# Kernel optimization log

Measured on AMD Instinct MI355X. Metric: run time of the kernel, lower is better.

The kernel has to match this reference:

```python
import jax, jax.numpy as jnp
import numpy as np

B = 128      # batch_size
TF = 80      # video_frame (encoder steps)
DEC = 30     # decoder_length
E = 512      # EmbeddingDim / LSTM hidden size
FEAT = 4096  # video feature dim
V = 6000     # total_words (vocab)


def setup_inputs() -> dict:
    key = jax.random.key(0)
    ks = jax.random.split(key, 13)
    s = 0.05  # weight init scale
    d = {
        "feat": jax.random.normal(ks[0], (B, TF, FEAT), jnp.float32),
        "caption": jax.random.normal(ks[1], (B, DEC, E), jnp.float32),
        "caption_one_hot": jax.random.uniform(ks[2], (B, DEC, V), jnp.float32),
        # LSTMCell 1: input 4096 -> hidden 512 (PyTorch gate order i,f,g,o)
        "w_ih1": jax.random.normal(ks[3], (4 * E, FEAT), jnp.float32) * s,
        "w_hh1": jax.random.normal(ks[4], (4 * E, E), jnp.float32) * s,
        "b_ih1": jax.random.normal(ks[5], (4 * E,), jnp.float32) * s,
        "b_hh1": jax.random.normal(ks[6], (4 * E,), jnp.float32) * s,
        # LSTMCell 2: input 2*512 -> hidden 512
        "w_ih2": jax.random.normal(ks[7], (4 * E, 2 * E), jnp.float32) * s,
        "w_hh2": jax.random.normal(ks[8], (4 * E, E), jnp.float32) * s,
        "b_ih2": jax.random.normal(ks[9], (4 * E,), jnp.float32) * s,
        "b_hh2": jax.random.normal(ks[10], (4 * E,), jnp.float32) * s,
        # output projection to vocab
        "w_out": jax.random.normal(ks[11], (V, E), jnp.float32) * s,
        "b_out": jax.random.normal(ks[12], (V,), jnp.float32) * s,
        "keep_rate": 10,  # coin >= keep_rate never true -> teacher forcing
    }
    return d


def _lstm_cell(x, h, c, w_ih, w_hh, b_ih, b_hh):
    # gates: [B, 4E]; PyTorch LSTMCell gate order (i, f, g, o)
    gates = x @ w_ih.T + h @ w_hh.T + b_ih + b_hh
    i, f, g, o = jnp.split(gates, 4, axis=1)
    c_new = jax.nn.sigmoid(f) * c + jax.nn.sigmoid(i) * jnp.tanh(g)
    h_new = jax.nn.sigmoid(o) * jnp.tanh(c_new)
    return h_new, c_new


def reference(feat, caption, caption_one_hot,
              w_ih1, w_hh1, b_ih1, b_hh1,
              w_ih2, w_hh2, b_ih2, b_hh2,
              w_out, b_out, keep_rate):
    dt = feat.dtype
    pad1 = jnp.zeros((B, FEAT), dt)  # padding_lstm1
    pad2 = jnp.zeros((B, E), dt)     # padding_lstm2

    def enc_step(carry, x):
        h1, c1, h2, c2 = carry
        h1, c1 = _lstm_cell(x, h1, c1, w_ih1, w_hh1, b_ih1, b_hh1)
        h2, c2 = _lstm_cell(jnp.concatenate([pad2, h1], axis=1),
                            h2, c2, w_ih2, w_hh2, b_ih2, b_hh2)
        return (h1, c1, h2, c2), None

    init = tuple(jnp.zeros((B, E), dt) for _ in range(4))
    carry, _ = jax.lax.scan(enc_step, init, jnp.swapaxes(feat, 0, 1))  # [TF,B,FEAT]

    # labels at step+1: argmax over vocab dim (torch.max(caption_one_hot,1)[1])
    labels = jnp.argmax(caption_one_hot, axis=2)  # [B, DEC]

    def dec_step(carry, inp):
        h1, c1, h2, c2 = carry
        x_word, lab = inp  # [B,E], [B]
        h1, c1 = _lstm_cell(pad1, h1, c1, w_ih1, w_hh1, b_ih1, b_hh1)
        h2, c2 = _lstm_cell(jnp.concatenate([x_word, h1], axis=1),
                            h2, c2, w_ih2, w_hh2, b_ih2, b_hh2)
        logits = h2 @ w_out.T + b_out  # [B, V]
        logp = jax.nn.log_softmax(logits, axis=1)
        step_loss = -jnp.take_along_axis(logp, lab[:, None], axis=1)[:, 0]
        return (h1, c1, h2, c2), jnp.sum(step_loss) / B

    xs = (jnp.swapaxes(caption[:, :DEC - 1, :], 0, 1),  # [DEC-1, B, E]
          jnp.swapaxes(labels[:, 1:DEC], 0, 1))         # [DEC-1, B]
    carry, losses = jax.lax.scan(dec_step, carry, xs)
    return jnp.sum(losses).reshape((1,))
```

## Files before the change

kernel.cpp:

```cpp
#include <hip/hip_runtime.h>
#include <cstdint>
#include <cstddef>

#define BB    128
#define TFRM  80
#define DECL  30
#define EE    512
#define FEATD 4096
#define VV    6000
#define VPAD  6016

using frag_ab = __attribute__((ext_vector_type(8))) short;
using frag_cd = __attribute__((ext_vector_type(4))) float;

static __device__ __forceinline__ float sigf(float x)  { return 1.0f / (1.0f + __expf(-x)); }
static __device__ __forceinline__ float tanhf_(float x){ float e = __expf(2.0f * x); return 1.0f - 2.0f / (e + 1.0f); }
static __device__ __forceinline__ unsigned short f2bf_rne(float x) {
    unsigned int u = __float_as_uint(x);
    u += 0x7fffu + ((u >> 16) & 1u);
    return (unsigned short)(u >> 16);
}

__global__ void init_zero(unsigned int* h1a, unsigned int* h1b, unsigned int* h2a, unsigned int* h2b,
                          float* c1, float* c2, float* out) {
    int i = blockIdx.x * blockDim.x + threadIdx.x;
    if (i < 32768) { h1a[i] = 0u; h1b[i] = 0u; h2a[i] = 0u; h2b[i] = 0u; }
    c1[i] = 0.f; c2[i] = 0.f;
    if (i == 0) out[0] = 0.f;
}

__global__ void f2bf(const float* __restrict__ src, unsigned short* __restrict__ dst, int n4) {
    int i = blockIdx.x * blockDim.x + threadIdx.x;
    if (i >= n4) return;
    float4 v = ((const float4*)src)[i];
    ushort4 o;
    o.x = f2bf_rne(v.x); o.y = f2bf_rne(v.y); o.z = f2bf_rne(v.z); o.w = f2bf_rne(v.w);
    ((ushort4*)dst)[i] = o;
}

__global__ void build_wcat2(const float* __restrict__ w_ih2, const float* __restrict__ w_hh2,
                            unsigned short* __restrict__ dst, int n4) {
    int i = blockIdx.x * blockDim.x + threadIdx.x;
    if (i >= n4) return;
    int r  = i >> 8;
    int c  = (i & 255) * 4;
    const float* src = (c < 512) ? (w_ih2 + (size_t)r * 1024 + 512 + c)
                                 : (w_hh2 + (size_t)r * 512 + (c - 512));
    float4 v = *(const float4*)src;
    ushort4 o;
    o.x = f2bf_rne(v.x); o.y = f2bf_rne(v.y); o.z = f2bf_rne(v.z); o.w = f2bf_rne(v.w);
    ((ushort4*)dst)[i] = o;
}

__global__ void wout_pad(const float* __restrict__ w_out, unsigned short* __restrict__ dst, int n4) {
    int i = blockIdx.x * blockDim.x + threadIdx.x;
    if (i >= n4) return;
    int r = i >> 7;
    int c = (i & 127) * 4;
    ushort4 o;
    if (r < VV) {
        float4 v = *(const float4*)(w_out + (size_t)r * EE + c);
        o.x = f2bf_rne(v.x); o.y = f2bf_rne(v.y); o.z = f2bf_rne(v.z); o.w = f2bf_rne(v.w);
    } else {
        o.x = 0; o.y = 0; o.z = 0; o.w = 0;
    }
    ((ushort4*)dst)[i] = o;
}

__global__ void xdec_gather(const float* __restrict__ cap, unsigned short* __restrict__ dst, int n4) {
    int i = blockIdx.x * blockDim.x + threadIdx.x;
    if (i >= n4) return;
    int row = i >> 7;
    int c   = (i & 127) * 4;
    int b = row / 29, t = row - b * 29;
    float4 v = *(const float4*)(cap + (size_t)(b * DECL + t) * EE + c);
    ushort4 o;
    o.x = f2bf_rne(v.x); o.y = f2bf_rne(v.y); o.z = f2bf_rne(v.z); o.w = f2bf_rne(v.w);
    ((ushort4*)dst)[i] = o;
}

__global__ void bias_sum(const float* b_ih1, const float* b_hh1, const float* b_ih2, const float* b_hh2,
                         float* bs1, float* bs2) {
    int i = blockIdx.x * blockDim.x + threadIdx.x;
    bs1[i] = b_ih1[i] + b_hh1[i];
    bs2[i] = b_ih2[i] + b_hh2[i];
}

__global__ void argmax_k(const float* __restrict__ oh, int* __restrict__ labels) {
    int row = blockIdx.x;
    const float* p = oh + (size_t)row * VV;
    int lane = threadIdx.x;
    float best = -1e30f; int bi = 0x7fffffff;
    for (int v = lane; v < VV; v += 64) {
        float x = p[v];
        if (x > best) { best = x; bi = v; }
    }
    for (int off = 32; off; off >>= 1) {
        float ob = __shfl_down(best, off);
        int   oi = __shfl_down(bi,   off);
        if (ob > best || (ob == best && oi < bi)) { best = ob; bi = oi; }
    }
    if (lane == 0) labels[row] = bi;
}

__global__ __launch_bounds__(256) void gemm64(const unsigned short* __restrict__ A, int lda,
                                              const unsigned short* __restrict__ B, int ldb,
                                              float* __restrict__ C, int ldc,
                                              int K, int ntiles,
                                              const float* __restrict__ bias, int biasN) {
    __shared__ unsigned short As[64][40];
    __shared__ unsigned short Bs[64][40];
    int bm = blockIdx.x / ntiles;
    int bn = blockIdx.x % ntiles;
    int tid = threadIdx.x;
    int wave = tid >> 6, lane = tid & 63;

    int srow  = tid >> 2;
    int scol8 = (tid & 3) * 8;
    const unsigned short* Ap = A + (size_t)(bm * 64 + srow) * lda + scol8;
    const unsigned short* Bp = B + (size_t)(bn * 64 + srow) * ldb + scol8;

    frag_cd acc[4] = {};
    int m16 = lane & 15, kg8 = (lane >> 4) * 8;

    for (int k0 = 0; k0 < K; k0 += 32) {
        *(uint4*)&As[srow][scol8] = *(const uint4*)(Ap + k0);
        *(uint4*)&Bs[srow][scol8] = *(const uint4*)(Bp + k0);
        __syncthreads();
        frag_ab bfrag = *(frag_ab*)&Bs[wave * 16 + m16][kg8];
        #pragma unroll
        for (int mt = 0; mt < 4; ++mt) {
            frag_ab afrag = *(frag_ab*)&As[mt * 16 + m16][kg8];
            acc[mt] = __builtin_amdgcn_mfma_f32_16x16x32_bf16(afrag, bfrag, acc[mt], 0, 0, 0);
        }
        __syncthreads();
    }
    int col = bn * 64 + wave * 16 + (lane & 15);
    float bv = 0.f;
    if (bias) bv = (col < biasN) ? bias[col] : 0.f;
    #pragma unroll
    for (int mt = 0; mt < 4; ++mt) {
        int rbase = bm * 64 + mt * 16 + (lane >> 4) * 4;
        #pragma unroll
        for (int i = 0; i < 4; ++i)
            C[(size_t)(rbase + i) * ldc + col] = acc[mt][i] + bv;
    }
}

__global__ __launch_bounds__(256) void lstm_step(const unsigned short* __restrict__ W, int K,
                                                 const unsigned short* __restrict__ Xa,
                                                 const unsigned short* __restrict__ Xb,
                                                 const float* __restrict__ P, int pstride,
                                                 const float* __restrict__ bias,
                                                 float* __restrict__ c,
                                                 unsigned short* __restrict__ hout) {
    __shared__ unsigned short Ws[64][136];
    __shared__ unsigned short Xs[16][136];
    __shared__ float gbuf[4][16][17];

    int et = blockIdx.x >> 3;
    int nt = blockIdx.x & 7;
    int e0 = et * 16, b0 = nt * 16;
    int tid = threadIdx.x;
    int wave = tid >> 6, lane = tid & 63;
    int m16 = lane & 15, kg8 = (lane >> 4) * 8;

    frag_cd acc = {};

    for (int k0 = 0; k0 < K; k0 += 128) {
        #pragma unroll
        for (int p = 0; p < 4; ++p) {
            int lr = p * 16 + (tid >> 4);
            int g = lr >> 4, ei = lr & 15;
            int col8 = (tid & 15) * 8;
            *(uint4*)&Ws[lr][col8] =
                *(const uint4*)(W + (size_t)(g * EE + e0 + ei) * K + k0 + col8);
        }
        {
            int r = tid >> 4;
            int col8 = (tid & 15) * 8;
            const unsigned short* src = (k0 < 512)
                ? (Xa + (size_t)(b0 + r) * EE + k0 + col8)
                : (Xb + (size_t)(b0 + r) * EE + (k0 - 512) + col8);
            *(uint4*)&Xs[r][col8] = *(const uint4*)src;
        }
        __syncthreads();
        #pragma unroll
        for (int kk = 0; kk < 4; ++kk) {
            frag_ab af = *(frag_ab*)&Ws[wave * 16 + m16][kk * 32 + kg8];
            frag_ab bf = *(frag_ab*)&Xs[m16][kk * 32 + kg8];
            acc = __builtin_amdgcn_mfma_f32_16x16x32_bf16(af, bf, acc, 0, 0, 0);
        }
        __syncthreads();
    }

    {
        int er = (lane >> 4) * 4, cb = lane & 15;
        #pragma unroll
        for (int i = 0; i < 4; ++i) gbuf[wave][er + i][cb] = acc[i];
    }
    __syncthreads();

    {
        int e = tid & 15, b = tid >> 4;
        int row = e0 + e;
        int bg  = b0 + b;
        float gi = gbuf[0][e][b] + bias[row];
        float gf = gbuf[1][e][b] + bias[EE + row];
        float gg = gbuf[2][e][b] + bias[2 * EE + row];
        float go = gbuf[3][e][b] + bias[3 * EE + row];
        if (P) {
            const float* pp = P + (size_t)bg * pstride;
            gi += pp[row]; gf += pp[EE + row]; gg += pp[2 * EE + row]; go += pp[3 * EE + row];
        }
        size_t cidx = (size_t)bg * EE + row;
        float cn = sigf(gf) * c[cidx] + sigf(gi) * tanhf_(gg);
        float hn = sigf(go) * tanhf_(cn);
        c[cidx] = cn;
        hout[(size_t)bg * EE + row] = f2bf_rne(hn);
    }
}

__global__ __launch_bounds__(256) void loss_reduce(const float* __restrict__ logits,
                                                   const int* __restrict__ labels,
                                                   int tcol, float* __restrict__ out) {
    __shared__ float red[256];
    int b = blockIdx.x, tid = threadIdx.x;
    const float* lg = logits + (size_t)b * VPAD;
    float mx = -1e30f;
    for (int v = tid; v < VV; v += 256) mx = fmaxf(mx, lg[v]);
    red[tid] = mx; __syncthreads();
    for (int s = 128; s; s >>= 1) {
        if (tid < s) red[tid] = fmaxf(red[tid], red[tid + s]);
        __syncthreads();
    }
    mx = red[0]; __syncthreads();
    float sm = 0.f;
    for (int v = tid; v < VV; v += 256) sm += __expf(lg[v] - mx);
    red[tid] = sm; __syncthreads();
    for (int s = 128; s; s >>= 1) {
        if (tid < s) red[tid] += red[tid + s];
        __syncthreads();
    }
    if (tid == 0) {
        int lab = labels[b * DECL + tcol];
        atomicAdd(out, (mx + __logf(red[0]) - lg[lab]) * (1.0f / BB));
    }
}

extern "C" void kernel_launch(void* const* d_in, const int* in_sizes, int n_in,
                              void* d_out, int out_size, void* d_ws, size_t ws_size,
                              hipStream_t stream) {
    const float* feat    = (const float*)d_in[0];
    const float* caption = (const float*)d_in[1];
    const float* onehot  = (const float*)d_in[2];
    const float* w_ih1   = (const float*)d_in[3];
    const float* w_hh1   = (const float*)d_in[4];
    const float* b_ih1   = (const float*)d_in[5];
    const float* b_hh1   = (const float*)d_in[6];
    const float* w_ih2   = (const float*)d_in[7];
    const float* w_hh2   = (const float*)d_in[8];
    const float* b_ih2   = (const float*)d_in[9];
    const float* b_hh2   = (const float*)d_in[10];
    const float* w_out   = (const float*)d_in[11];
    const float* b_out   = (const float*)d_in[12];
    float* out = (float*)d_out;

    char* ws = (char*)d_ws;
    size_t off = 0;
    auto alloc = [&](size_t bytes) -> char* {
        char* p = ws + off;
        off = (off + bytes + 255) & ~(size_t)255;
        return p;
    };
    unsigned short* feat_bf  = (unsigned short*)alloc((size_t)BB * TFRM * FEATD * 2);
    unsigned short* wih1_bf  = (unsigned short*)alloc((size_t)2048 * FEATD * 2);
    unsigned short* wih2_bf  = (unsigned short*)alloc((size_t)2048 * 1024 * 2);
    unsigned short* whh1_bf  = (unsigned short*)alloc((size_t)2048 * EE * 2);
    unsigned short* wcat2_bf = (unsigned short*)alloc((size_t)2048 * 1024 * 2);
    unsigned short* wout_bf  = (unsigned short*)alloc((size_t)VPAD * EE * 2);
    float* P_enc = (float*)alloc((size_t)BB * TFRM * 2048 * 4);
    float* P_dec = (float*)alloc((size_t)BB * 29 * 2048 * 4);
    unsigned short* xdec_bf = (unsigned short*)alloc((size_t)BB * 29 * EE * 2);
    unsigned short* h1a = (unsigned short*)alloc((size_t)BB * EE * 2);
    unsigned short* h1b = (unsigned short*)alloc((size_t)BB * EE * 2);
    unsigned short* h2a = (unsigned short*)alloc((size_t)BB * EE * 2);
    unsigned short* h2b = (unsigned short*)alloc((size_t)BB * EE * 2);
    float* C1 = (float*)alloc((size_t)BB * EE * 4);
    float* C2 = (float*)alloc((size_t)BB * EE * 4);
    float* logits = (float*)alloc((size_t)BB * VPAD * 4);
    float* bias1 = (float*)alloc(2048 * 4);
    float* bias2 = (float*)alloc(2048 * 4);
    int* labels = (int*)alloc((size_t)BB * DECL * 4);
    if (off > ws_size) return;

    init_zero<<<256, 256, 0, stream>>>((unsigned int*)h1a, (unsigned int*)h1b,
                                       (unsigned int*)h2a, (unsigned int*)h2b, C1, C2, out);
    f2bf<<<40960, 256, 0, stream>>>(feat, feat_bf, BB * TFRM * FEATD / 4);
    f2bf<<<8192, 256, 0, stream>>>(w_ih1, wih1_bf, 2048 * FEATD / 4);
    f2bf<<<2048, 256, 0, stream>>>(w_ih2, wih2_bf, 2048 * 1024 / 4);
    f2bf<<<1024, 256, 0, stream>>>(w_hh1, whh1_bf, 2048 * EE / 4);
    build_wcat2<<<2048, 256, 0, stream>>>(w_ih2, w_hh2, wcat2_bf, 2048 * 1024 / 4);
    wout_pad<<<3008, 256, 0, stream>>>(w_out, wout_bf, VPAD * EE / 4);
    xdec_gather<<<1856, 256, 0, stream>>>(caption, xdec_bf, BB * 29 * EE / 4);
    bias_sum<<<8, 256, 0, stream>>>(b_ih1, b_hh1, b_ih2, b_hh2, bias1, bias2);
    argmax_k<<<BB * DECL, 64, 0, stream>>>(onehot, labels);

    gemm64<<<160 * 32, 256, 0, stream>>>(feat_bf, FEATD, wih1_bf, FEATD, P_enc, 2048,
                                         FEATD, 32, nullptr, 0);
    gemm64<<<58 * 32, 256, 0, stream>>>(xdec_bf, EE, wih2_bf, 1024, P_dec, 2048,
                                        EE, 32, nullptr, 0);

    unsigned short *h1c = h1a, *h1n = h1b, *h2c = h2a, *h2n = h2b;
    for (int t = 0; t < TFRM; ++t) {
        lstm_step<<<256, 256, 0, stream>>>(whh1_bf, EE, h1c, nullptr,
                                           P_enc + (size_t)t * 2048, TFRM * 2048,
                                           bias1, C1, h1n);
        { unsigned short* tmp = h1c; h1c = h1n; h1n = tmp; }
        lstm_step<<<256, 256, 0, stream>>>(wcat2_bf, 1024, h1c, h2c, nullptr, 0,
                                           bias2, C2, h2n);
        { unsigned short* tmp = h2c; h2c = h2n; h2n = tmp; }
    }
    for (int t = 0; t < DECL - 1; ++t) {
        lstm_step<<<256, 256, 0, stream>>>(whh1_bf, EE, h1c, nullptr, nullptr, 0,
                                           bias1, C1, h1n);
        { unsigned short* tmp = h1c; h1c = h1n; h1n = tmp; }
        lstm_step<<<256, 256, 0, stream>>>(wcat2_bf, 1024, h1c, h2c,
                                           P_dec + (size_t)t * 2048, 29 * 2048,
                                           bias2, C2, h2n);
        { unsigned short* tmp = h2c; h2c = h2n; h2n = tmp; }
        gemm64<<<2 * 94, 256, 0, stream>>>(h2c, EE, wout_bf, EE, logits, VPAD,
                                           EE, 94, b_out, VV);
        loss_reduce<<<BB, 256, 0, stream>>>(logits, labels, t + 1, out);
    }
}
```

Measured before the change: 3.060 ms.

## Fuse LSTM recurrence into one persistent kernel with grid barriers

Replaces the roughly 300 per-step kernel launches of the encoder and decoder recurrence, the output projection and the loss with a single persistent kernel of 256 blocks that synchronises through an atomic grid barrier. Weights and hidden states are pre-swizzled into MFMA fragment order so each wave reads fragments straight from global memory without LDS staging. The next step's layer-1 cell and the previous step's loss are overlapped with the logits and layer-2 phases. This relies on all 256 blocks being co-resident and adds spin-wait barrier cost in place of launch overhead.

```diff
diff --git a/kernel.cpp b/kernel.cpp
--- a/kernel.cpp
+++ b/kernel.cpp
@@ -22,11 +22,11 @@
 }
 
 __global__ void init_zero(unsigned int* h1a, unsigned int* h1b, unsigned int* h2a, unsigned int* h2b,
-                          float* c1, float* c2, float* out) {
+                          float* c1, float* c2, float* out, int* bar) {
     int i = blockIdx.x * blockDim.x + threadIdx.x;
     if (i < 32768) { h1a[i] = 0u; h1b[i] = 0u; h2a[i] = 0u; h2b[i] = 0u; }
     c1[i] = 0.f; c2[i] = 0.f;
-    if (i == 0) out[0] = 0.f;
+    if (i == 0) { out[0] = 0.f; bar[0] = 0; bar[1] = 0; }
 }
 
 __global__ void f2bf(const float* __restrict__ src, unsigned short* __restrict__ dst, int n4) {
@@ -38,33 +38,32 @@
     ((ushort4*)dst)[i] = o;
 }
 
-__global__ void build_wcat2(const float* __restrict__ w_ih2, const float* __restrict__ w_hh2,
-                            unsigned short* __restrict__ dst, int n4) {
-    int i = blockIdx.x * blockDim.x + threadIdx.x;
-    if (i >= n4) return;
-    int r  = i >> 8;
-    int c  = (i & 255) * 4;
-    const float* src = (c < 512) ? (w_ih2 + (size_t)r * 1024 + 512 + c)
-                                 : (w_hh2 + (size_t)r * 512 + (c - 512));
-    float4 v = *(const float4*)src;
-    ushort4 o;
-    o.x = f2bf_rne(v.x); o.y = f2bf_rne(v.y); o.z = f2bf_rne(v.z); o.w = f2bf_rne(v.w);
-    ((ushort4*)dst)[i] = o;
-}
-
-__global__ void wout_pad(const float* __restrict__ w_out, unsigned short* __restrict__ dst, int n4) {
-    int i = blockIdx.x * blockDim.x + threadIdx.x;
-    if (i >= n4) return;
-    int r = i >> 7;
-    int c = (i & 127) * 4;
-    ushort4 o;
-    if (r < VV) {
-        float4 v = *(const float4*)(w_out + (size_t)r * EE + c);
-        o.x = f2bf_rne(v.x); o.y = f2bf_rne(v.y); o.z = f2bf_rne(v.z); o.w = f2bf_rne(v.w);
-    } else {
-        o.x = 0; o.y = 0; o.z = 0; o.w = 0;
-    }
-    ((ushort4*)dst)[i] = o;
+__global__ void wsw_hh(const float* __restrict__ W, unsigned short* __restrict__ dst) {
+    int i = blockIdx.x * blockDim.x + threadIdx.x;
+    int j = i & 7, lane = (i >> 3) & 63, t = i >> 9;
+    int kf = t & 15, r16 = t >> 4;
+    int row = r16 * 16 + (lane & 15);
+    int k = kf * 32 + ((lane >> 4) << 3) + j;
+    dst[i] = f2bf_rne(W[(size_t)row * 512 + k]);
+}
+__global__ void wsw_cat(const float* __restrict__ w_ih2, const float* __restrict__ w_hh2,
+                        unsigned short* __restrict__ dst) {
+    int i = blockIdx.x * blockDim.x + threadIdx.x;
+    int j = i & 7, lane = (i >> 3) & 63, t = i >> 9;
+    int kf = t & 31, r16 = t >> 5;
+    int row = r16 * 16 + (lane & 15);
+    int k = kf * 32 + ((lane >> 4) << 3) + j;
+    float v = (k < 512) ? w_ih2[(size_t)row * 1024 + 512 + k]
+                        : w_hh2[(size_t)row * 512 + (k - 512)];
+    dst[i] = f2bf_rne(v);
+}
+__global__ void wsw_out(const float* __restrict__ w_out, unsigned short* __restrict__ dst) {
+    int i = blockIdx.x * blockDim.x + threadIdx.x;
+    int j = i & 7, lane = (i >> 3) & 63, t = i >> 9;
+    int kf = t & 15, r16 = t >> 4;
+    int row = r16 * 16 + (lane & 15);
+    int k = kf * 32 + ((lane >> 4) << 3) + j;
+    dst[i] = (row < VV) ? f2bf_rne(w_out[(size_t)row * 512 + k]) : (unsigned short)0;
 }
 
 __global__ void xdec_gather(const float* __restrict__ cap, unsigned short* __restrict__ dst, int n4) {
@@ -106,8 +105,7 @@
 __global__ __launch_bounds__(256) void gemm64(const unsigned short* __restrict__ A, int lda,
                                               const unsigned short* __restrict__ B, int ldb,
                                               float* __restrict__ C, int ldc,
-                                              int K, int ntiles,
-                                              const float* __restrict__ bias, int biasN) {
+                                              int K, int ntiles) {
     __shared__ unsigned short As[64][40];
     __shared__ unsigned short Bs[64][40];
     int bm = blockIdx.x / ntiles;
@@ -136,75 +134,80 @@
         __syncthreads();
     }
     int col = bn * 64 + wave * 16 + (lane & 15);
-    float bv = 0.f;
-    if (bias) bv = (col < biasN) ? bias[col] : 0.f;
     #pragma unroll
     for (int mt = 0; mt < 4; ++mt) {
         int rbase = bm * 64 + mt * 16 + (lane >> 4) * 4;
         #pragma unroll
         for (int i = 0; i < 4; ++i)
-            C[(size_t)(rbase + i) * ldc + col] = acc[mt][i] + bv;
-    }
-}
-
-__global__ __launch_bounds__(256) void lstm_step(const unsigned short* __restrict__ W, int K,
-                                                 const unsigned short* __restrict__ Xa,
-                                                 const unsigned short* __restrict__ Xb,
-                                                 const float* __restrict__ P, int pstride,
-                                                 const float* __restrict__ bias,
-                                                 float* __restrict__ c,
-                                                 unsigned short* __restrict__ hout) {
-    __shared__ unsigned short Ws[64][136];
-    __shared__ unsigned short Xs[16][136];
-    __shared__ float gbuf[4][16][17];
-
-    int et = blockIdx.x >> 3;
-    int nt = blockIdx.x & 7;
-    int e0 = et * 16, b0 = nt * 16;
-    int tid = threadIdx.x;
-    int wave = tid >> 6, lane = tid & 63;
-    int m16 = lane & 15, kg8 = (lane >> 4) * 8;
-
+            C[(size_t)(rbase + i) * ldc + col] = acc[mt][i];
+    }
+}
+
+struct MegaArgs {
+    const unsigned short *whh1, *wcat2, *wout;
+    const float *bias1, *bias2, *b_out;
+    const float *P_enc, *P_dec;
+    unsigned short *h1a, *h1b, *h2a, *h2b;
+    float *c1, *c2;
+    float *logits;
+    const int *labels;
+    float *out;
+    int *bar;
+};
+
+#define NGRID 256
+
+static __device__ __forceinline__ void gsync(int* bar, int& mygen) {
+    __syncthreads();
+    if (threadIdx.x == 0) {
+        __threadfence();
+        mygen++;
+        int t = __hip_atomic_fetch_add(&bar[0], 1, __ATOMIC_ACQ_REL, __HIP_MEMORY_SCOPE_AGENT);
+        if (t == NGRID - 1) {
+            __hip_atomic_store(&bar[0], 0, __ATOMIC_RELAXED, __HIP_MEMORY_SCOPE_AGENT);
+            __hip_atomic_store(&bar[1], mygen, __ATOMIC_RELEASE, __HIP_MEMORY_SCOPE_AGENT);
+        } else {
+            while (__hip_atomic_load(&bar[1], __ATOMIC_ACQUIRE, __HIP_MEMORY_SCOPE_AGENT) < mygen) {
+                __builtin_amdgcn_s_sleep(2);
+            }
+        }
+        __threadfence();
+    }
+    __syncthreads();
+}
+
+template<int KF>
+static __device__ __forceinline__ void cell_phase(
+    const unsigned short* __restrict__ Wsw,
+    const unsigned short* __restrict__ Xa,
+    const unsigned short* __restrict__ Xb,
+    const float* __restrict__ P, int pstride,
+    const float* __restrict__ bias,
+    float* __restrict__ c, unsigned short* __restrict__ hout,
+    int et, int bt, float (&gbuf)[4][16][17])
+{
+    const int tid = threadIdx.x;
+    const int w = tid >> 6, lane = tid & 63;
+    const unsigned short* Ap = Wsw + ((size_t)(w * 32 + et) * KF) * 512 + lane * 8;
+    const unsigned short* Ba = Xa + (size_t)bt * 8192 + lane * 8;
+    const unsigned short* Bb = Xb ? Xb + (size_t)bt * 8192 + lane * 8 : (const unsigned short*)0;
     frag_cd acc = {};
-
-    for (int k0 = 0; k0 < K; k0 += 128) {
-        #pragma unroll
-        for (int p = 0; p < 4; ++p) {
-            int lr = p * 16 + (tid >> 4);
-            int g = lr >> 4, ei = lr & 15;
-            int col8 = (tid & 15) * 8;
-            *(uint4*)&Ws[lr][col8] =
-                *(const uint4*)(W + (size_t)(g * EE + e0 + ei) * K + k0 + col8);
-        }
-        {
-            int r = tid >> 4;
-            int col8 = (tid & 15) * 8;
-            const unsigned short* src = (k0 < 512)
-                ? (Xa + (size_t)(b0 + r) * EE + k0 + col8)
-                : (Xb + (size_t)(b0 + r) * EE + (k0 - 512) + col8);
-            *(uint4*)&Xs[r][col8] = *(const uint4*)src;
-        }
-        __syncthreads();
-        #pragma unroll
-        for (int kk = 0; kk < 4; ++kk) {
-            frag_ab af = *(frag_ab*)&Ws[wave * 16 + m16][kk * 32 + kg8];
-            frag_ab bf = *(frag_ab*)&Xs[m16][kk * 32 + kg8];
-            acc = __builtin_amdgcn_mfma_f32_16x16x32_bf16(af, bf, acc, 0, 0, 0);
-        }
-        __syncthreads();
-    }
-
+    #pragma unroll
+    for (int kf = 0; kf < KF; ++kf) {
+        frag_ab af = *(const frag_ab*)(Ap + kf * 512);
+        frag_ab bf = (kf < 16) ? *(const frag_ab*)(Ba + kf * 512)
+                               : *(const frag_ab*)(Bb + (kf - 16) * 512);
+        acc = __builtin_amdgcn_mfma_f32_16x16x32_bf16(af, bf, acc, 0, 0, 0);
+    }
     {
         int er = (lane >> 4) * 4, cb = lane & 15;
         #pragma unroll
-        for (int i = 0; i < 4; ++i) gbuf[wave][er + i][cb] = acc[i];
+        for (int i = 0; i < 4; ++i) gbuf[w][er + i][cb] = acc[i];
     }
     __syncthreads();
-
     {
         int e = tid & 15, b = tid >> 4;
-        int row = e0 + e;
-        int bg  = b0 + b;
+        int row = et * 16 + e, bg = bt * 16 + b;
         float gi = gbuf[0][e][b] + bias[row];
         float gf = gbuf[1][e][b] + bias[EE + row];
         float gg = gbuf[2][e][b] + bias[2 * EE + row];
@@ -213,18 +216,51 @@
             const float* pp = P + (size_t)bg * pstride;
             gi += pp[row]; gf += pp[EE + row]; gg += pp[2 * EE + row]; go += pp[3 * EE + row];
         }
-        size_t cidx = (size_t)bg * EE + row;
-        float cn = sigf(gf) * c[cidx] + sigf(gi) * tanhf_(gg);
+        size_t ci = (size_t)bg * EE + row;
+        float cn = sigf(gf) * c[ci] + sigf(gi) * tanhf_(gg);
         float hn = sigf(go) * tanhf_(cn);
-        c[cidx] = cn;
-        hout[(size_t)bg * EE + row] = f2bf_rne(hn);
-    }
-}
-
-__global__ __launch_bounds__(256) void loss_reduce(const float* __restrict__ logits,
-                                                   const int* __restrict__ labels,
-                                                   int tcol, float* __restrict__ out) {
-    __shared__ float red[256];
+        c[ci] = cn;
+        int kf = row >> 5, kj = row & 31;
+        int slane = b + ((kj >> 3) << 4);
+        hout[(size_t)bt * 8192 + kf * 512 + slane * 8 + (kj & 7)] = f2bf_rne(hn);
+    }
+    __syncthreads();
+}
+
+static __device__ __forceinline__ void logits_phase(
+    const unsigned short* __restrict__ Wosw, const unsigned short* __restrict__ h2sw,
+    const float* __restrict__ b_out, float* __restrict__ logits, int et, int bt)
+{
+    int tid = threadIdx.x, w = tid >> 6, lane = tid & 63;
+    frag_ab hb[16];
+    const unsigned short* Bp = h2sw + (size_t)bt * 8192 + lane * 8;
+    #pragma unroll
+    for (int kf = 0; kf < 16; ++kf) hb[kf] = *(const frag_ab*)(Bp + kf * 512);
+    for (int j = 0; j < 3; ++j) {
+        int vt = et * 4 + w + 128 * j;
+        if (vt >= VPAD / 16) break;
+        const unsigned short* Ap = Wosw + (size_t)vt * 8192 + lane * 8;
+        frag_cd acc = {};
+        #pragma unroll
+        for (int kf = 0; kf < 16; ++kf) {
+            frag_ab af = *(const frag_ab*)(Ap + kf * 512);
+            acc = __builtin_amdgcn_mfma_f32_16x16x32_bf16(af, hb[kf], acc, 0, 0, 0);
+        }
+        int col = bt * 16 + (lane & 15);
+        int r0 = vt * 16 + (lane >> 4) * 4;
+        #pragma unroll
+        for (int i = 0; i < 4; ++i) {
+            int vrow = r0 + i;
+            float bv = (vrow < VV) ? b_out[vrow] : 0.0f;
+            logits[(size_t)col * VPAD + vrow] = acc[i] + bv;
+        }
+    }
+}
+
+static __device__ __forceinline__ void loss_phase(
+    const float* __restrict__ logits, const int* __restrict__ labels,
+    int tcol, float* __restrict__ out, float (&red)[256])
+{
     int b = blockIdx.x, tid = threadIdx.x;
     const float* lg = logits + (size_t)b * VPAD;
     float mx = -1e30f;
@@ -246,6 +282,46 @@
         int lab = labels[b * DECL + tcol];
         atomicAdd(out, (mx + __logf(red[0]) - lg[lab]) * (1.0f / BB));
     }
+    __syncthreads();
+}
+
+__global__ __launch_bounds__(256, 1) void recurrence_k(MegaArgs a) {
+    __shared__ float gbuf[4][16][17];
+    __shared__ float red[256];
+    const int et = blockIdx.x >> 3, bt = blockIdx.x & 7;
+    int mygen = 0;
+
+    unsigned short *h1r = a.h1a, *h1w = a.h1b, *h2r = a.h2a, *h2w = a.h2b;
+
+    for (int t = 0; t < TFRM; ++t) {
+        cell_phase<16>(a.whh1, h1r, nullptr, a.P_enc + (size_t)t * 2048, TFRM * 2048,
+                       a.bias1, a.c1, h1w, et, bt, gbuf);
+        gsync(a.bar, mygen);
+        cell_phase<32>(a.wcat2, h1w, h2r, nullptr, 0,
+                       a.bias2, a.c2, h2w, et, bt, gbuf);
+        { unsigned short* tmp = h1r; h1r = h1w; h1w = tmp; }
+        { unsigned short* tmp = h2r; h2r = h2w; h2w = tmp; }
+        gsync(a.bar, mygen);
+    }
+
+    cell_phase<16>(a.whh1, h1r, nullptr, nullptr, 0, a.bias1, a.c1, h1w, et, bt, gbuf);
+    { unsigned short* tmp = h1r; h1r = h1w; h1w = tmp; }
+    gsync(a.bar, mygen);
+
+    for (int t = 0; t < DECL - 1; ++t) {
+        cell_phase<32>(a.wcat2, h1r, h2r, a.P_dec + (size_t)t * 2048, (DECL - 1) * 2048,
+                       a.bias2, a.c2, h2w, et, bt, gbuf);
+        if (t > 0 && blockIdx.x < BB) loss_phase(a.logits, a.labels, t, a.out, red);
+        { unsigned short* tmp = h2r; h2r = h2w; h2w = tmp; }
+        gsync(a.bar, mygen);
+        logits_phase(a.wout, h2r, a.b_out, a.logits, et, bt);
+        if (t < DECL - 2) {
+            cell_phase<16>(a.whh1, h1r, nullptr, nullptr, 0, a.bias1, a.c1, h1w, et, bt, gbuf);
+            { unsigned short* tmp = h1r; h1r = h1w; h1w = tmp; }
+        }
+        gsync(a.bar, mygen);
+    }
+    if (blockIdx.x < BB) loss_phase(a.logits, a.labels, DECL - 1, a.out, red);
 }
 
 extern "C" void kernel_launch(void* const* d_in, const int* in_sizes, int n_in,
@@ -276,12 +352,12 @@
     unsigned short* feat_bf  = (unsigned short*)alloc((size_t)BB * TFRM * FEATD * 2);
     unsigned short* wih1_bf  = (unsigned short*)alloc((size_t)2048 * FEATD * 2);
     unsigned short* wih2_bf  = (unsigned short*)alloc((size_t)2048 * 1024 * 2);
-    unsigned short* whh1_bf  = (unsigned short*)alloc((size_t)2048 * EE * 2);
-    unsigned short* wcat2_bf = (unsigned short*)alloc((size_t)2048 * 1024 * 2);
-    unsigned short* wout_bf  = (unsigned short*)alloc((size_t)VPAD * EE * 2);
+    unsigned short* whh1_sw  = (unsigned short*)alloc((size_t)2048 * EE * 2);
+    unsigned short* wcat2_sw = (unsigned short*)alloc((size_t)2048 * 1024 * 2);
+    unsigned short* wout_sw  = (unsigned short*)alloc((size_t)VPAD * EE * 2);
     float* P_enc = (float*)alloc((size_t)BB * TFRM * 2048 * 4);
-    float* P_dec = (float*)alloc((size_t)BB * 29 * 2048 * 4);
-    unsigned short* xdec_bf = (unsigned short*)alloc((size_t)BB * 29 * EE * 2);
+    float* P_dec = (float*)alloc((size_t)BB * (DECL - 1) * 2048 * 4);
+    unsigned short* xdec_bf = (unsigned short*)alloc((size_t)BB * (DECL - 1) * EE * 2);
     unsigned short* h1a = (unsigned short*)alloc((size_t)BB * EE * 2);
     unsigned short* h1b = (unsigned short*)alloc((size_t)BB * EE * 2);
     unsigned short* h2a = (unsigned short*)alloc((size_t)BB * EE * 2);
@@ -292,45 +368,33 @@
     float* bias1 = (float*)alloc(2048 * 4);
     float* bias2 = (float*)alloc(2048 * 4);
     int* labels = (int*)alloc((size_t)BB * DECL * 4);
+    int* bar    = (int*)alloc(256);
     if (off > ws_size) return;
 
     init_zero<<<256, 256, 0, stream>>>((unsigned int*)h1a, (unsigned int*)h1b,
-                                       (unsigned int*)h2a, (unsigned int*)h2b, C1, C2, out);
+                                       (unsigned int*)h2a, (unsigned int*)h2b, C1, C2, out, bar);
     f2bf<<<40960, 256, 0, stream>>>(feat, feat_bf, BB * TFRM * FEATD / 4);
     f2bf<<<8192, 256, 0, stream>>>(w_ih1, wih1_bf, 2048 * FEATD / 4);
     f2bf<<<2048, 256, 0, stream>>>(w_ih2, wih2_bf, 2048 * 1024 / 4);
-    f2bf<<<1024, 256, 0, stream>>>(w_hh1, whh1_bf, 2048 * EE / 4);
-    build_wcat2<<<2048, 256, 0, stream>>>(w_ih2, w_hh2, wcat2_bf, 2048 * 1024 / 4);
-    wout_pad<<<3008, 256, 0, stream>>>(w_out, wout_bf, VPAD * EE / 4);
-    xdec_gather<<<1856, 256, 0, stream>>>(caption, xdec_bf, BB * 29 * EE / 4);
+    wsw_hh<<<4096, 256, 0, stream>>>(w_hh1, whh1_sw);
+    wsw_cat<<<8192, 256, 0, stream>>>(w_ih2, w_hh2, wcat2_sw);
+    wsw_out<<<12032, 256, 0, stream>>>(w_out, wout_sw);
+    xdec_gather<<<1856, 256, 0, stream>>>(caption, xdec_bf, BB * (DECL - 1) * EE / 4);
     bias_sum<<<8, 256, 0, stream>>>(b_ih1, b_hh1, b_ih2, b_hh2, bias1, bias2);
     argmax_k<<<BB * DECL, 64, 0, stream>>>(onehot, labels);
 
     gemm64<<<160 * 32, 256, 0, stream>>>(feat_bf, FEATD, wih1_bf, FEATD, P_enc, 2048,
-                                         FEATD, 32, nullptr, 0);
+                                         FEATD, 32);
     gemm64<<<58 * 32, 256, 0, stream>>>(xdec_bf, EE, wih2_bf, 1024, P_dec, 2048,
-                                        EE, 32, nullptr, 0);
-
-    unsigned short *h1c = h1a, *h1n = h1b, *h2c = h2a, *h2n = h2b;
-    for (int t = 0; t < TFRM; ++t) {
-        lstm_step<<<256, 256, 0, stream>>>(whh1_bf, EE, h1c, nullptr,
-                                           P_enc + (size_t)t * 2048, TFRM * 2048,
-                                           bias1, C1, h1n);
-        { unsigned short* tmp = h1c; h1c = h1n; h1n = tmp; }
-        lstm_step<<<256, 256, 0, stream>>>(wcat2_bf, 1024, h1c, h2c, nullptr, 0,
-                                           bias2, C2, h2n);
-        { unsigned short* tmp = h2c; h2c = h2n; h2n = tmp; }
-    }
-    for (int t = 0; t < DECL - 1; ++t) {
-        lstm_step<<<256, 256, 0, stream>>>(whh1_bf, EE, h1c, nullptr, nullptr, 0,
-                                           bias1, C1, h1n);
-        { unsigned short* tmp = h1c; h1c = h1n; h1n = tmp; }
-        lstm_step<<<256, 256, 0, stream>>>(wcat2_bf, 1024, h1c, h2c,
-                                           P_dec + (size_t)t * 2048, 29 * 2048,
-                                           bias2, C2, h2n);
-        { unsigned short* tmp = h2c; h2c = h2n; h2n = tmp; }
-        gemm64<<<2 * 94, 256, 0, stream>>>(h2c, EE, wout_bf, EE, logits, VPAD,
-                                           EE, 94, b_out, VV);
-        loss_reduce<<<BB, 256, 0, stream>>>(logits, labels, t + 1, out);
-    }
-}
+                                        EE, 32);
+
+    MegaArgs ka;
+    ka.whh1 = whh1_sw; ka.wcat2 = wcat2_sw; ka.wout = wout_sw;
+    ka.bias1 = bias1; ka.bias2 = bias2; ka.b_out = b_out;
+    ka.P_enc = P_enc; ka.P_dec = P_dec;
+    ka.h1a = h1a; ka.h1b = h1b; ka.h2a = h2a; ka.h2b = h2b;
+    ka.c1 = C1; ka.c2 = C2;
+    ka.logits = logits; ka.labels = labels; ka.out = out;
+    ka.bar = bar;
+    recurrence_k<<<NGRID, 256, 0, stream>>>(ka);
+}
```

New measurement: 9.469 ms. +209.5%, slower.
